# Kernel optimization log

Hardware: AMD Instinct MI355X
Metric: run time of the kernel (lower is better)

The kernel has to match this reference:

```python
import jax, jax.numpy as jnp
import numpy as np

N = 20000      # nodes
E = 640000     # edges (before self loops)
IN = 256       # in_channels == out_channels (forced by classifier size 4*in)
H1, C1 = 8, 16   # conv1: heads=8, out=16 -> concat 128
H2, C2 = 1, 256  # conv2: heads=1, out=out_channels
B = 4096       # article pairs
NEG_SLOPE = 0.2  # PyG GATv2Conv default negative_slope


def setup_inputs() -> dict:
    key = jax.random.key(0)
    ks = jax.random.split(key, 24)
    s = 0.05
    inp = {
        "gnn_x": jax.random.normal(ks[0], (N, IN), jnp.float32),
        "vanilla_x": jax.random.normal(ks[1], (N, IN), jnp.float32),
        "edge_src": jax.random.randint(ks[2], (E,), 0, N, jnp.int32),
        "edge_dst": jax.random.randint(ks[3], (E,), 0, N, jnp.int32),
        "a1_idx": jax.random.randint(ks[4], (B,), 0, N, jnp.int64),
        "a2_idx": jax.random.randint(ks[5], (B,), 0, N, jnp.int64),
        # conv1 params (lin_l, lin_r, att, bias)
        "Wl1": jax.random.normal(ks[6], (IN, H1 * C1), jnp.float32) * s,
        "bl1": jnp.zeros((H1 * C1,), jnp.float32),
        "Wr1": jax.random.normal(ks[7], (IN, H1 * C1), jnp.float32) * s,
        "br1": jnp.zeros((H1 * C1,), jnp.float32),
        "att1": jax.random.normal(ks[8], (H1, C1), jnp.float32) * s,
        "bias1": jnp.zeros((H1 * C1,), jnp.float32),
        # conv2 params
        "Wl2": jax.random.normal(ks[9], (H1 * C1, H2 * C2), jnp.float32) * s,
        "bl2": jnp.zeros((H2 * C2,), jnp.float32),
        "Wr2": jax.random.normal(ks[10], (H1 * C1, H2 * C2), jnp.float32) * s,
        "br2": jnp.zeros((H2 * C2,), jnp.float32),
        "att2": jax.random.normal(ks[11], (H2, C2), jnp.float32) * s,
        "bias2": jnp.zeros((H2 * C2,), jnp.float32),
        # classifier
        "Wc": jax.random.normal(ks[12], (4 * IN, 1), jnp.float32) * s,
        "bc": jnp.zeros((1,), jnp.float32),
    }
    return inp


def _gatv2_layer(x, src, dst, Wl, bl, Wr, br, att, bias):
    """GATv2Conv: x_l = lin_l(x)[src], x_r = lin_r(x)[dst];
    e = att . leaky_relu(x_l + x_r); segment softmax over dst; scatter-add x_l*alpha."""
    n = x.shape[0]
    h, c = att.shape
    xl = (x @ Wl + bl).reshape(n, h, c)
    xr = (x @ Wr + br).reshape(n, h, c)
    # per-edge attention logits [E, H]
    e = jnp.einsum('ehc,hc->eh', jax.nn.leaky_relu(xl[src] + xr[dst], NEG_SLOPE), att)
    # segment softmax over destination nodes (self loops guarantee non-empty segments)
    emax = jax.ops.segment_max(e, dst, num_segments=n)
    ex = jnp.exp(e - emax[dst])
    denom = jax.ops.segment_sum(ex, dst, num_segments=n)
    alpha = ex / denom[dst]                      # [E, H]
    out = jax.ops.segment_sum(alpha[:, :, None] * xl[src], dst, num_segments=n)  # [N,H,C]
    return out.reshape(n, h * c) + bias          # concat=True (heads=1 identical)


def reference(gnn_x, vanilla_x, Wl1, bl1, Wr1, br1, att1, bias1,
              Wl2, bl2, Wr2, br2, att2, bias2, Wc, bc,
              edge_src, edge_dst, a1_idx, a2_idx):
    n = gnn_x.shape[0]
    loops = jnp.arange(n, dtype=edge_src.dtype)
    src = jnp.concatenate([edge_src, loops])     # PyG add_self_loops=True
    dst = jnp.concatenate([edge_dst, loops])
    x = _gatv2_layer(gnn_x, src, dst, Wl1, bl1, Wr1, br1, att1, bias1)
    x = jax.nn.relu(x)
    x = _gatv2_layer(x, src, dst, Wl2, bl2, Wr2, br2, att2, bias2)
    combined = jnp.concatenate(
        [vanilla_x[a1_idx], vanilla_x[a2_idx], x[a1_idx], x[a2_idx]], axis=1)  # [B, 4*IN]
    logits = combined @ Wc + bc                  # [B, 1]
    return logits
```

## Files before the change

kernel.cpp:

```cpp
#include <hip/hip_runtime.h>
#include <math.h>

#define N_NODES 20000
#define M_PAD   20032
#define E_EDGES 640000
#define ET (E_EDGES + N_NODES)
#define IN_CH 256
#define D1 128
#define D2 256
#define BPAIRS 4096
#define NEG 0.2f
#define LOG2E 1.4426950408889634f

#define NB_HIST   128
#define CHUNK     ((ET + NB_HIST - 1) / NB_HIST)
#define HALF_BINS 10000

#define WT_BLOCKS    32
#define ZC_BLOCKS    20
#define XCONV_BLOCKS (M_PAD * IN_CH / 4 / 4 / 256)
#define PREP_BLOCKS  (NB_HIST + WT_BLOCKS + ZC_BLOCKS + XCONV_BLOCKS)

#define RP_BLOCKS ((N_NODES + 255) / 256)

#define G1X (M_PAD / 64)
#define G1Y (D1 / 64)
#define G1_BLOCKS (G1X * G1Y)
#define SCAT_BLOCKS ((ET + 255) / 256)

#if __has_builtin(__builtin_amdgcn_exp2f)
#define EXP2F(x) __builtin_amdgcn_exp2f(x)
#else
#define EXP2F(x) exp2f(x)
#endif

typedef __bf16 bf16x8 __attribute__((ext_vector_type(8)));
typedef float  f32x4  __attribute__((ext_vector_type(4)));
typedef float  f32x2  __attribute__((ext_vector_type(2)));
typedef unsigned short u16x4 __attribute__((ext_vector_type(4)));

__device__ __forceinline__ unsigned short f2b(float f) {
    unsigned int u = __float_as_uint(f);
    unsigned int r = u + 0x7FFFu + ((u >> 16) & 1u);
    return (unsigned short)(r >> 16);
}
__device__ __forceinline__ unsigned char f2f8(float f) {
    return (unsigned char)(__builtin_amdgcn_cvt_pk_fp8_f32(f, f, 0, false) & 0xFF);
}
template <bool HI>
__device__ __forceinline__ f32x2 f8up2(unsigned int u) {
    return __builtin_amdgcn_cvt_pk_f32_fp8((int)u, HI);
}
__device__ __forceinline__ f32x2 up2(unsigned int u) {
    f32x2 r;
    r.x = __uint_as_float(u << 16);
    r.y = __uint_as_float(u & 0xFFFF0000u);
    return r;
}
__device__ __forceinline__ f32x2 lrelu2(f32x2 s) {
    return __builtin_elementwise_max(s, s * NEG);
}
__device__ __forceinline__ float lrelu(float s) { return fmaxf(s, NEG * s); }

__device__ __forceinline__ void unpack8(uint4 u, float* v) {
    v[0] = __uint_as_float(u.x << 16); v[1] = __uint_as_float(u.x & 0xFFFF0000u);
    v[2] = __uint_as_float(u.y << 16); v[3] = __uint_as_float(u.y & 0xFFFF0000u);
    v[4] = __uint_as_float(u.z << 16); v[5] = __uint_as_float(u.z & 0xFFFF0000u);
    v[6] = __uint_as_float(u.w << 16); v[7] = __uint_as_float(u.w & 0xFFFF0000u);
}
__device__ __forceinline__ void unpack8_f8(uint2 u, float* v) {
    f32x2 a = f8up2<false>(u.x), b = f8up2<true>(u.x);
    f32x2 c = f8up2<false>(u.y), d = f8up2<true>(u.y);
    v[0] = a.x; v[1] = a.y; v[2] = b.x; v[3] = b.y;
    v[4] = c.x; v[5] = c.y; v[6] = d.x; v[7] = d.y;
}


__global__ __launch_bounds__(256) void prep_kernel(
        const float* __restrict__ gnn_x,
        const float* __restrict__ Wl1, const float* __restrict__ Wr1,
        const float* __restrict__ Wl2, const float* __restrict__ Wr2,
        const int* __restrict__ edge_dst,
        unsigned short* __restrict__ xb,
        unsigned short* __restrict__ wt1l, unsigned short* __restrict__ wt1r,
        unsigned short* __restrict__ wt2l, unsigned short* __restrict__ wt2r,
        int* __restrict__ cb,
        int* __restrict__ rank,
        int* __restrict__ ibuf) {
    __shared__ int lc[HALF_BINS];
    int bid = blockIdx.x;
    if (bid < NB_HIST) {
        int ebeg = bid * CHUNK;
        int eend = min(ebeg + CHUNK, ET);
#pragma unroll 1
        for (int half = 0; half < 2; half++) {
            int lo = half * HALF_BINS;
            for (int i = threadIdx.x; i < HALF_BINS; i += 256) lc[i] = 0;
            __syncthreads();
            for (int e = ebeg + threadIdx.x; e < eend; e += 256) {
                int dst = (e < E_EDGES) ? edge_dst[e] : (e - E_EDGES);
                int d = dst - lo;
                if (0 <= d && d < HALF_BINS) rank[e] = atomicAdd(&lc[d], 1);
            }
            __syncthreads();
            for (int i = threadIdx.x; i < HALF_BINS; i += 256)
                cb[(size_t)bid * N_NODES + lo + i] = lc[i];
            __syncthreads();
        }
    } else if (bid < NB_HIST + WT_BLOCKS) {
        unsigned short* tile = (unsigned short*)lc;
        int t = bid - NB_HIST;
        int m = t >> 3;
        int tt = t & 7;
        const float* W;
        unsigned short* Wt;
        int K, N;
        if (m == 0)      { W = Wl1; Wt = wt1l; K = IN_CH; N = D1; }
        else if (m == 1) { W = Wr1; Wt = wt1r; K = IN_CH; N = D1; }
        else if (m == 2) { W = Wl2; Wt = wt2l; K = D1; N = D2; }
        else             { W = Wr2; Wt = wt2r; K = D1; N = D2; }
        int ntn = N >> 6;
        int k0 = (tt / ntn) << 6;
        int n0 = (tt % ntn) << 6;
        int c = threadIdx.x & 63;
        int rr = threadIdx.x >> 6;
#pragma unroll
        for (int ch = 0; ch < 16; ch++) {
            int row = rr * 16 + ch;
            tile[row * 65 + c] = f2b(W[(size_t)(k0 + row) * N + n0 + c]);
        }
        __syncthreads();
#pragma unroll
        for (int ch = 0; ch < 16; ch++) {
            int n = rr * 16 + ch;
            Wt[(size_t)(n0 + n) * K + k0 + c] = tile[c * 65 + n];
        }
    } else if (bid < NB_HIST + WT_BLOCKS + ZC_BLOCKS) {
        int q = (bid - NB_HIST - WT_BLOCKS) * 256 + threadIdx.x;
        int4 z; z.x = z.y = z.z = z.w = 0;
        ((int4*)ibuf)[q] = z;
    } else {
        int tid = (bid - NB_HIST - WT_BLOCKS - ZC_BLOCKS) * 256 + threadIdx.x;
        const int NQ = M_PAD * IN_CH / 4;
        int q0 = tid * 4;
#pragma unroll
        for (int j = 0; j < 4; j++) {
            int qi = q0 + j;
            if (qi >= NQ) break;
            int e0 = qi * 4;
            int row = e0 >> 8;
            u16x4 o;
            if (row < N_NODES) {
                f32x4 v = __builtin_nontemporal_load((const f32x4*)(gnn_x + e0));
                o.x = f2b(v.x); o.y = f2b(v.y); o.z = f2b(v.z); o.w = f2b(v.w);
            } else {
                o.x = o.y = o.z = o.w = 0;
            }
            *(u16x4*)(xb + e0) = o;
        }
    }
}

__device__ __forceinline__ void scan256(const int* __restrict__ count,
                                        int* __restrict__ offsets,
                                        int* wbuf) {
    const int PER = 79;
    int t = threadIdx.x;
    int base = t * PER;
    int v[PER];
#pragma unroll
    for (int i = 0; i < PER; i++) {
        int idx = base + i;
        v[i] = (idx < N_NODES) ? count[idx] : 0;
    }
    int sum = 0;
#pragma unroll
    for (int i = 0; i < PER; i++) sum += v[i];
    int lane = t & 63, wave = t >> 6;
    int s = sum;
#pragma unroll
    for (int off = 1; off < 64; off <<= 1) {
        int x = __shfl_up(s, off);
        if (lane >= off) s += x;
    }
    int* wsum = wbuf;
    int* wpre = wbuf + 4;
    if (lane == 63) wsum[wave] = s;
    __syncthreads();
    if (t == 0) {
        int acc = 0;
        for (int w = 0; w < 4; w++) { wpre[w] = acc; acc += wsum[w]; }
    }
    __syncthreads();
    int excl = wpre[wave] + (s - sum);
    if (t == 255) offsets[N_NODES] = excl + sum;
    int run = excl;
#pragma unroll
    for (int i = 0; i < PER; i++) {
        int idx = base + i;
        if (idx < N_NODES) { offsets[idx] = run; run += v[i]; }
    }
}


__global__ __launch_bounds__(256) void repprefix_scan_kernel(
        int* __restrict__ cb, int* __restrict__ count,
        int* __restrict__ done, int* __restrict__ offsets) {
    __shared__ int wbuf[8];
    __shared__ int islast;
    int dst = blockIdx.x * 256 + threadIdx.x;
    if (dst < N_NODES) {
        int v[NB_HIST];
#pragma unroll
        for (int r = 0; r < NB_HIST; r++)
            v[r] = cb[(size_t)r * N_NODES + dst];
        int run = 0;
#pragma unroll
        for (int r = 0; r < NB_HIST; r++) {
            int c = v[r];
            v[r] = run;
            run += c;
        }
#pragma unroll
        for (int r = 0; r < NB_HIST; r++)
            cb[(size_t)r * N_NODES + dst] = v[r];
        atomicAdd(&count[dst], run);
    }
    __builtin_amdgcn_s_waitcnt(0);
    __syncthreads();
    if (threadIdx.x == 0) {
        int old = __hip_atomic_fetch_add(done, 1, __ATOMIC_RELAXED,
                                         __HIP_MEMORY_SCOPE_AGENT);
        islast = (old == RP_BLOCKS - 1) ? 1 : 0;
    }
    __syncthreads();
    if (islast) {
        scan256(count, offsets, wbuf);
    }
}


template <int K>
__device__ __forceinline__ void dual_gemm_tile(
        const unsigned short* __restrict__ A,
        const unsigned short* __restrict__ Wtl,
        const unsigned short* __restrict__ Wtr,
        const float* __restrict__ bl, const float* __restrict__ br,
        unsigned char* __restrict__ Yl, unsigned short* __restrict__ Yr,
        int M, int NOUT, int bx, int by) {
    const int NK = K / 32;
    int wave = threadIdx.x >> 6;
    int lane = threadIdx.x & 63;
    int row0 = bx * 64;
    int col0 = (by * 4 + wave) * 16;
    int rsub = lane & 15;
    int koff = (lane >> 4) * 8;

    const unsigned short* ap  = A   + (size_t)(row0 + rsub) * K + koff;
    const unsigned short* bpl = Wtl + (size_t)(col0 + rsub) * K + koff;
    const unsigned short* bpr = Wtr + (size_t)(col0 + rsub) * K + koff;

    bf16x8 bfl[NK], bfr[NK];
#pragma unroll
    for (int kb = 0; kb < NK; kb++) {
        bfl[kb] = *(const bf16x8*)(bpl + kb * 32);
        bfr[kb] = *(const bf16x8*)(bpr + kb * 32);
    }

    f32x4 l0 = {0.f, 0.f, 0.f, 0.f};
    f32x4 l1 = l0, l2 = l0, l3 = l0, r0 = l0, r1 = l0, r2 = l0, r3 = l0;

#pragma unroll
    for (int kb = 0; kb < NK; kb++) {
        int off = kb * 32;
        bf16x8 a0 = *(const bf16x8*)(ap + off);
        bf16x8 a1 = *(const bf16x8*)(ap + 16 * K + off);
        bf16x8 a2 = *(const bf16x8*)(ap + 32 * K + off);
        bf16x8 a3 = *(const bf16x8*)(ap + 48 * K + off);
        l0 = __builtin_amdgcn_mfma_f32_16x16x32_bf16(a0, bfl[kb], l0, 0, 0, 0);
        r0 = __builtin_amdgcn_mfma_f32_16x16x32_bf16(a0, bfr[kb], r0, 0, 0, 0);
        l1 = __builtin_amdgcn_mfma_f32_16x16x32_bf16(a1, bfl[kb], l1, 0, 0, 0);
        r1 = __builtin_amdgcn_mfma_f32_16x16x32_bf16(a1, bfr[kb], r1, 0, 0, 0);
        l2 = __builtin_amdgcn_mfma_f32_16x16x32_bf16(a2, bfl[kb], l2, 0, 0, 0);
        r2 = __builtin_amdgcn_mfma_f32_16x16x32_bf16(a2, bfr[kb], r2, 0, 0, 0);
        l3 = __builtin_amdgcn_mfma_f32_16x16x32_bf16(a3, bfl[kb], l3, 0, 0, 0);
        r3 = __builtin_amdgcn_mfma_f32_16x16x32_bf16(a3, bfr[kb], r3, 0, 0, 0);
    }

    int colg = col0 + rsub;
    float bvl = bl[colg];
    float bvr = br[colg];
    int rbase = row0 + (lane >> 4) * 4;
#pragma unroll
    for (int t = 0; t < 4; t++) {
        f32x4 al = (t == 0) ? l0 : (t == 1) ? l1 : (t == 2) ? l2 : l3;
        f32x4 ar = (t == 0) ? r0 : (t == 1) ? r1 : (t == 2) ? r2 : r3;
#pragma unroll
        for (int r = 0; r < 4; r++) {
            int row = rbase + t * 16 + r;
            if (row < M) {
                Yl[(size_t)row * NOUT + colg] = f2f8(al[r] + bvl);
                Yr[(size_t)row * NOUT + colg] = f2b(ar[r] + bvr);
            }
        }
    }
}


__global__ __launch_bounds__(256) void gemm1_scatter_kernel(
        const unsigned short* __restrict__ A,
        const unsigned short* __restrict__ Wtl,
        const unsigned short* __restrict__ Wtr,
        const float* __restrict__ bl, const float* __restrict__ br,
        unsigned char* __restrict__ Yl, unsigned short* __restrict__ Yr,
        const int* __restrict__ edge_src, const int* __restrict__ edge_dst,
        const int* __restrict__ rank, const int* __restrict__ offsets,
        const int* __restrict__ cb, int* __restrict__ sorted_src) {
    int bid = blockIdx.x;
    if (bid < G1_BLOCKS) {
        dual_gemm_tile<IN_CH>(A, Wtl, Wtr, bl, br, Yl, Yr,
                              N_NODES, D1, bid % G1X, bid / G1X);
    } else {
        int e = (bid - G1_BLOCKS) * 256 + threadIdx.x;
        if (e >= ET) return;
        int dst = (e < E_EDGES) ? edge_dst[e] : (e - E_EDGES);
        int src = (e < E_EDGES) ? edge_src[e] : (e - E_EDGES);
        int rep = e / CHUNK;
        sorted_src[offsets[dst] + cb[(size_t)rep * N_NODES + dst] + rank[e]] = src;
    }
}


__global__ __launch_bounds__(256) void aggregate1_kernel(
        const unsigned char* __restrict__ xl1, const unsigned short* __restrict__ xr1,
        const float* __restrict__ att1, const float* __restrict__ bias1,
        const int* __restrict__ offsets, const int* __restrict__ sorted_src,
        unsigned short* __restrict__ x1) {
    int wave = threadIdx.x >> 6;
    int lane = threadIdx.x & 63;
    int q = lane >> 4;
    int ql = lane & 15;
    int dst = blockIdx.x * 4 + wave;
    if (dst >= M_PAD) return;
    int c0 = ql * 8;
    if (dst >= N_NODES) {
        if (q == 0) {
            uint4 z; z.x = z.y = z.z = z.w = 0;
            *(uint4*)(x1 + (size_t)dst * D1 + c0) = z;
        }
        return;
    }

    uint4 xu = *(const uint4*)(xr1 + (size_t)dst * D1 + c0);
    f32x2 xr[4] = {up2(xu.x), up2(xu.y), up2(xu.z), up2(xu.w)};
    float4 aa0 = *(const float4*)(att1 + c0);
    float4 aa1 = *(const float4*)(att1 + c0 + 4);
    f32x2 att[4];
    att[0].x = aa0.x * LOG2E; att[0].y = aa0.y * LOG2E;
    att[1].x = aa0.z * LOG2E; att[1].y = aa0.w * LOG2E;
    att[2].x = aa1.x * LOG2E; att[2].y = aa1.y * LOG2E;
    att[3].x = aa1.z * LOG2E; att[3].y = aa1.w * LOG2E;

    int beg = offsets[dst], end = offsets[dst + 1];
    const unsigned char* base = xl1 + c0;

    float l = 0.f;
    f32x2 acc[4] = {{0.f,0.f},{0.f,0.f},{0.f,0.f},{0.f,0.f}};

    int i = beg;
    int s0 = sorted_src[min(i + q, end - 1)];
    uint2 g0 = *(const uint2*)(base + (size_t)s0 * D1);
    bool more1 = (i + 4) < end;
    uint2 g1;
    if (more1) {
        int s1 = sorted_src[min(i + 4 + q, end - 1)];
        g1 = *(const uint2*)(base + (size_t)s1 * D1);
    }
    while (true) {
        bool more2 = (i + 8) < end;
        uint2 g2;
        if (more2) {
            int s2 = sorted_src[min(i + 8 + q, end - 1)];
            g2 = *(const uint2*)(base + (size_t)s2 * D1);
        }
        bool act = (i + q) < end;
        f32x2 v0 = f8up2<false>(g0.x), v1 = f8up2<true>(g0.x);
        f32x2 v2 = f8up2<false>(g0.y), v3 = f8up2<true>(g0.y);
        f32x2 p2 = att[0] * lrelu2(v0 + xr[0]);
        p2 += att[1] * lrelu2(v1 + xr[1]);
        p2 += att[2] * lrelu2(v2 + xr[2]);
        p2 += att[3] * lrelu2(v3 + xr[3]);
        float p = p2.x + p2.y;
        p += __shfl_xor(p, 1);
        float w = act ? EXP2F(p) : 0.f;
        l += w;
        acc[0] += w * v0; acc[1] += w * v1; acc[2] += w * v2; acc[3] += w * v3;
        if (!more1) break;
        i += 4;
        g0 = g1; g1 = g2; more1 = more2;
    }
    l += __shfl_xor(l, 16);
    l += __shfl_xor(l, 32);
#pragma unroll
    for (int j = 0; j < 4; j++) {
        f32x2 t;
        t.x = __shfl_xor(acc[j].x, 16); t.y = __shfl_xor(acc[j].y, 16);
        acc[j] += t;
        t.x = __shfl_xor(acc[j].x, 32); t.y = __shfl_xor(acc[j].y, 32);
        acc[j] += t;
    }
    if (q == 0) {
        float inv = 1.f / l;
        float4 bb0 = *(const float4*)(bias1 + c0);
        float4 bb1 = *(const float4*)(bias1 + c0 + 4);
        unsigned short o[8];
        o[0] = f2b(fmaxf(acc[0].x * inv + bb0.x, 0.f));
        o[1] = f2b(fmaxf(acc[0].y * inv + bb0.y, 0.f));
        o[2] = f2b(fmaxf(acc[1].x * inv + bb0.z, 0.f));
        o[3] = f2b(fmaxf(acc[1].y * inv + bb0.w, 0.f));
        o[4] = f2b(fmaxf(acc[2].x * inv + bb1.x, 0.f));
        o[5] = f2b(fmaxf(acc[2].y * inv + bb1.y, 0.f));
        o[6] = f2b(fmaxf(acc[3].x * inv + bb1.z, 0.f));
        o[7] = f2b(fmaxf(acc[3].y * inv + bb1.w, 0.f));
        uint4 ov;
        ov.x = (unsigned int)o[0] | ((unsigned int)o[1] << 16);
        ov.y = (unsigned int)o[2] | ((unsigned int)o[3] << 16);
        ov.z = (unsigned int)o[4] | ((unsigned int)o[5] << 16);
        ov.w = (unsigned int)o[6] | ((unsigned int)o[7] << 16);
        *(uint4*)(x1 + (size_t)dst * D1 + c0) = ov;
    }
}


template <int K>
__global__ __launch_bounds__(256) void dual_gemm_w32_kernel(
        const unsigned short* __restrict__ A,
        const unsigned short* __restrict__ Wtl,
        const unsigned short* __restrict__ Wtr,
        const float* __restrict__ bl, const float* __restrict__ br,
        unsigned char* __restrict__ Yl, unsigned short* __restrict__ Yr,
        int M, int NOUT) {
    const int NK = K / 32;
    int wave = threadIdx.x >> 6;
    int lane = threadIdx.x & 63;
    int row0 = blockIdx.x * 64;
    int col0 = blockIdx.y * 128 + wave * 32;
    int rsub = lane & 15;
    int koff = (lane >> 4) * 8;

    const unsigned short* ap = A + (size_t)(row0 + rsub) * K + koff;

    bf16x8 bfl[2][NK], bfr[2][NK];
#pragma unroll
    for (int c = 0; c < 2; c++) {
        const unsigned short* bpl = Wtl + (size_t)(col0 + c * 16 + rsub) * K + koff;
        const unsigned short* bpr = Wtr + (size_t)(col0 + c * 16 + rsub) * K + koff;
#pragma unroll
        for (int kb = 0; kb < NK; kb++) {
            bfl[c][kb] = *(const bf16x8*)(bpl + kb * 32);
            bfr[c][kb] = *(const bf16x8*)(bpr + kb * 32);
        }
    }

    f32x4 accl[2][4], accr[2][4];
#pragma unroll
    for (int c = 0; c < 2; c++)
#pragma unroll
        for (int t = 0; t < 4; t++) {
            accl[c][t] = (f32x4){0.f, 0.f, 0.f, 0.f};
            accr[c][t] = (f32x4){0.f, 0.f, 0.f, 0.f};
        }

#pragma unroll
    for (int kb = 0; kb < NK; kb++) {
        int off = kb * 32;
        bf16x8 a[4];
        a[0] = *(const bf16x8*)(ap + off);
        a[1] = *(const bf16x8*)(ap + 16 * K + off);
        a[2] = *(const bf16x8*)(ap + 32 * K + off);
        a[3] = *(const bf16x8*)(ap + 48 * K + off);
#pragma unroll
        for (int t = 0; t < 4; t++) {
#pragma unroll
            for (int c = 0; c < 2; c++) {
                accl[c][t] = __builtin_amdgcn_mfma_f32_16x16x32_bf16(
                    a[t], bfl[c][kb], accl[c][t], 0, 0, 0);
                accr[c][t] = __builtin_amdgcn_mfma_f32_16x16x32_bf16(
                    a[t], bfr[c][kb], accr[c][t], 0, 0, 0);
            }
        }
    }

    int rbase = row0 + (lane >> 4) * 4;
#pragma unroll
    for (int c = 0; c < 2; c++) {
        int colg = col0 + c * 16 + rsub;
        float bvl = bl[colg];
        float bvr = br[colg];
#pragma unroll
        for (int t = 0; t < 4; t++) {
#pragma unroll
            for (int r = 0; r < 4; r++) {
                int row = rbase + t * 16 + r;
                if (row < M) {
                    Yl[(size_t)row * NOUT + colg] = f2f8(accl[c][t][r] + bvl);
                    Yr[(size_t)row * NOUT + colg] = f2b(accr[c][t][r] + bvr);
                }
            }
        }
    }
}


__global__ __launch_bounds__(256) void agg2_classifier_kernel(
        const unsigned char* __restrict__ xl2, const unsigned short* __restrict__ xr2,
        const float* __restrict__ att2, const float* __restrict__ bias2,
        const int* __restrict__ offsets, const int* __restrict__ sorted_src,
        const float* __restrict__ vanilla_x,
        const int* __restrict__ a1_raw, const int* __restrict__ a2_raw,
        const float* __restrict__ Wc, const float* __restrict__ bc,
        float* __restrict__ out) {
    __shared__ float x2row[2][D2];
    __shared__ float mrg[2][32][9];
    __shared__ float part[4];
    __shared__ int stride_s;
    int t = threadIdx.x;
    if (t < 64) {
        bool z = (t < 31) ? (a1_raw[1 + 2 * t] == 0) : true;
        unsigned long long m = __ballot(z);
        if (t == 0) stride_s = (m == ~0ull) ? 2 : 1;
    }
    __syncthreads();
    int stride = stride_s;
    int b = blockIdx.x;
    int a1 = a1_raw[(long)b * stride];
    int a2 = a2_raw[(long)b * stride];

    int wave = t >> 6;
    int d = wave >> 1;
    int ww = wave & 1;
    int lane = t & 63;
    int half = lane >> 5;
    int hl = lane & 31;
    int c0 = hl * 8;
    int dst = d ? a2 : a1;

    float xr[8], att[8];
    unpack8(*(const uint4*)(xr2 + (size_t)dst * D2 + c0), xr);
#pragma unroll
    for (int j = 0; j < 8; j++) att[j] = att2[c0 + j] * LOG2E;
    int beg = offsets[dst], end = offsets[dst + 1];
    const unsigned char* base = xl2 + c0;

    float l = 0.f;
    float acc[8];
#pragma unroll
    for (int j = 0; j < 8; j++) acc[j] = 0.f;

    int sub = 2 * ww + half;
    int i = beg;
    int s0 = sorted_src[min(i + sub, end - 1)];
    uint2 g0 = *(const uint2*)(base + (size_t)s0 * D2);
    bool more1 = (i + 4) < end;
    uint2 g1;
    if (more1) {
        int s1 = sorted_src[min(i + 4 + sub, end - 1)];
        g1 = *(const uint2*)(base + (size_t)s1 * D2);
    }
    while (true) {
        bool more2 = (i + 8) < end;
        uint2 g2;
        if (more2) {
            int s2 = sorted_src[min(i + 8 + sub, end - 1)];
            g2 = *(const uint2*)(base + (size_t)s2 * D2);
        }
        bool act = (i + sub) < end;
        float v[8];
        unpack8_f8(g0, v);
        float p = 0.f;
#pragma unroll
        for (int j = 0; j < 8; j++) p = fmaf(att[j], lrelu(v[j] + xr[j]), p);
        p += __shfl_xor(p, 1);
        p += __shfl_xor(p, 2);
        p += __shfl_xor(p, 4);
        p += __shfl_xor(p, 8);
        p += __shfl_xor(p, 16);
        float w = act ? EXP2F(p) : 0.f;
        l += w;
#pragma unroll
        for (int j = 0; j < 8; j++) acc[j] += w * v[j];
        if (!more1) break;
        i += 4;
        g0 = g1; g1 = g2; more1 = more2;
    }
    l += __shfl_xor(l, 32);
#pragma unroll
    for (int j = 0; j < 8; j++) acc[j] += __shfl_xor(acc[j], 32);
    if (ww == 1 && half == 0) {
        mrg[d][hl][0] = l;
#pragma unroll
        for (int j = 0; j < 8; j++) mrg[d][hl][1 + j] = acc[j];
    }
    __syncthreads();
    if (ww == 0 && half == 0) {
        l += mrg[d][hl][0];
#pragma unroll
        for (int j = 0; j < 8; j++) acc[j] += mrg[d][hl][1 + j];
        float inv = 1.f / l;
#pragma unroll
        for (int j = 0; j < 8; j++)
            x2row[d][c0 + j] = acc[j] * inv + bias2[c0 + j];
    }
    __syncthreads();

    float s = vanilla_x[(size_t)a1 * IN_CH + t] * Wc[t]
            + vanilla_x[(size_t)a2 * IN_CH + t] * Wc[IN_CH + t]
            + x2row[0][t] * Wc[2 * IN_CH + t]
            + x2row[1][t] * Wc[3 * IN_CH + t];
    s += __shfl_xor(s, 1);
    s += __shfl_xor(s, 2);
    s += __shfl_xor(s, 4);
    s += __shfl_xor(s, 8);
    s += __shfl_xor(s, 16);
    s += __shfl_xor(s, 32);
    if (lane == 0) part[wave] = s;
    __syncthreads();
    if (t == 0) out[b] = part[0] + part[1] + part[2] + part[3] + bc[0];
}


extern "C" void kernel_launch(void* const* d_in, const int* in_sizes, int n_in,
                              void* d_out, int out_size, void* d_ws, size_t ws_size,
                              hipStream_t stream) {
    const float* gnn_x     = (const float*)d_in[0];
    const float* vanilla_x = (const float*)d_in[1];
    const int*   edge_src  = (const int*)d_in[2];
    const int*   edge_dst  = (const int*)d_in[3];
    const int*   a1_idx    = (const int*)d_in[4];
    const int*   a2_idx    = (const int*)d_in[5];
    const float* Wl1   = (const float*)d_in[6];
    const float* bl1   = (const float*)d_in[7];
    const float* Wr1   = (const float*)d_in[8];
    const float* br1   = (const float*)d_in[9];
    const float* att1  = (const float*)d_in[10];
    const float* bias1 = (const float*)d_in[11];
    const float* Wl2   = (const float*)d_in[12];
    const float* bl2   = (const float*)d_in[13];
    const float* Wr2   = (const float*)d_in[14];
    const float* br2   = (const float*)d_in[15];
    const float* att2  = (const float*)d_in[16];
    const float* bias2 = (const float*)d_in[17];
    const float* Wc    = (const float*)d_in[18];
    const float* bc    = (const float*)d_in[19];
    float* out = (float*)d_out;

    char* p = (char*)d_ws;
    unsigned short* xb   = (unsigned short*)p; p += (size_t)M_PAD * IN_CH * 2;
    unsigned short* x1b  = (unsigned short*)p; p += (size_t)M_PAD * D1 * 2;
    unsigned char*  xl1b = (unsigned char*)p;  p += (size_t)N_NODES * D1;
    unsigned short* xr1b = (unsigned short*)p; p += (size_t)N_NODES * D1 * 2;
    unsigned char*  xl2b = (unsigned char*)p;  p += (size_t)N_NODES * D2;
    unsigned short* xr2b = (unsigned short*)p; p += (size_t)N_NODES * D2 * 2;
    unsigned short* wt1l = (unsigned short*)p; p += (size_t)D1 * IN_CH * 2;
    unsigned short* wt1r = (unsigned short*)p; p += (size_t)D1 * IN_CH * 2;
    unsigned short* wt2l = (unsigned short*)p; p += (size_t)D2 * D1 * 2;
    unsigned short* wt2r = (unsigned short*)p; p += (size_t)D2 * D1 * 2;
    int* ibuf       = (int*)p; p += (size_t)20480 * 4;
    int* offsets    = (int*)p; p += (size_t)(N_NODES + 4) * 4;
    int* rank       = (int*)p; p += (size_t)ET * 4;
    int* sorted_src = (int*)p; p += (size_t)ET * 4;
    int* cb         = (int*)p; p += (size_t)NB_HIST * N_NODES * 4;
    int* count = ibuf;
    int* done  = ibuf + 20032;

    prep_kernel<<<PREP_BLOCKS, 256, 0, stream>>>(
        gnn_x, Wl1, Wr1, Wl2, Wr2, edge_dst,
        xb, wt1l, wt1r, wt2l, wt2r, cb, rank, ibuf);

    repprefix_scan_kernel<<<RP_BLOCKS, 256, 0, stream>>>(
        cb, count, done, offsets);

    gemm1_scatter_kernel<<<G1_BLOCKS + SCAT_BLOCKS, 256, 0, stream>>>(
        xb, wt1l, wt1r, bl1, br1, xl1b, xr1b,
        edge_src, edge_dst, rank, offsets, cb, sorted_src);

    aggregate1_kernel<<<M_PAD / 4, 256, 0, stream>>>(
        xl1b, xr1b, att1, bias1, offsets, sorted_src, x1b);

    dim3 g2(M_PAD / 64, D2 / 128);
    dual_gemm_w32_kernel<D1><<<g2, 256, 0, stream>>>(
        x1b, wt2l, wt2r, bl2, br2, xl2b, xr2b, N_NODES, D2);

    agg2_classifier_kernel<<<BPAIRS, 256, 0, stream>>>(
        xl2b, xr2b, att2, bias2, offsets, sorted_src,
        vanilla_x, a1_idx, a2_idx, Wc, bc, out);
}
```

Measured before the change: 256.3 us.

## Split histogram halves across blocks and use two waves per node in aggregate1

The histogram phase of the prep kernel now gives each half of the destination bin range its own block, which doubles the block count and removes the serial two-pass loop. The layer-1 aggregation now assigns two waves to each destination node. Each wave processes an interleaved half of the edges, and the partial sums are merged through shared memory after a block barrier. Both changes expose more parallelism and shorten the per-node dependency chain. The cost is that edge_dst is read twice across blocks, plus extra shared-memory traffic and a __syncthreads in the aggregation.

```diff
diff --git a/kernel.cpp b/kernel.cpp
--- a/kernel.cpp
+++ b/kernel.cpp
@@ -15,11 +15,12 @@
 #define NB_HIST   128
 #define CHUNK     ((ET + NB_HIST - 1) / NB_HIST)
 #define HALF_BINS 10000
+#define HIST_BLOCKS (NB_HIST * 2)
 
 #define WT_BLOCKS    32
 #define ZC_BLOCKS    20
 #define XCONV_BLOCKS (M_PAD * IN_CH / 4 / 4 / 256)
-#define PREP_BLOCKS  (NB_HIST + WT_BLOCKS + ZC_BLOCKS + XCONV_BLOCKS)
+#define PREP_BLOCKS  (HIST_BLOCKS + WT_BLOCKS + ZC_BLOCKS + XCONV_BLOCKS)
 
 #define RP_BLOCKS ((N_NODES + 255) / 256)
 
@@ -89,27 +90,25 @@
         int* __restrict__ ibuf) {
     __shared__ int lc[HALF_BINS];
     int bid = blockIdx.x;
-    if (bid < NB_HIST) {
-        int ebeg = bid * CHUNK;
+    if (bid < HIST_BLOCKS) {
+        int chunk = bid >> 1;
+        int half  = bid & 1;
+        int ebeg = chunk * CHUNK;
         int eend = min(ebeg + CHUNK, ET);
-#pragma unroll 1
-        for (int half = 0; half < 2; half++) {
-            int lo = half * HALF_BINS;
-            for (int i = threadIdx.x; i < HALF_BINS; i += 256) lc[i] = 0;
-            __syncthreads();
-            for (int e = ebeg + threadIdx.x; e < eend; e += 256) {
-                int dst = (e < E_EDGES) ? edge_dst[e] : (e - E_EDGES);
-                int d = dst - lo;
-                if (0 <= d && d < HALF_BINS) rank[e] = atomicAdd(&lc[d], 1);
-            }
-            __syncthreads();
-            for (int i = threadIdx.x; i < HALF_BINS; i += 256)
-                cb[(size_t)bid * N_NODES + lo + i] = lc[i];
-            __syncthreads();
-        }
-    } else if (bid < NB_HIST + WT_BLOCKS) {
+        int lo = half * HALF_BINS;
+        for (int i = threadIdx.x; i < HALF_BINS; i += 256) lc[i] = 0;
+        __syncthreads();
+        for (int e = ebeg + threadIdx.x; e < eend; e += 256) {
+            int dst = (e < E_EDGES) ? edge_dst[e] : (e - E_EDGES);
+            int d = dst - lo;
+            if (0 <= d && d < HALF_BINS) rank[e] = atomicAdd(&lc[d], 1);
+        }
+        __syncthreads();
+        for (int i = threadIdx.x; i < HALF_BINS; i += 256)
+            cb[(size_t)chunk * N_NODES + lo + i] = lc[i];
+    } else if (bid < HIST_BLOCKS + WT_BLOCKS) {
         unsigned short* tile = (unsigned short*)lc;
-        int t = bid - NB_HIST;
+        int t = bid - HIST_BLOCKS;
         int m = t >> 3;
         int tt = t & 7;
         const float* W;
@@ -135,12 +134,12 @@
             int n = rr * 16 + ch;
             Wt[(size_t)(n0 + n) * K + k0 + c] = tile[c * 65 + n];
         }
-    } else if (bid < NB_HIST + WT_BLOCKS + ZC_BLOCKS) {
-        int q = (bid - NB_HIST - WT_BLOCKS) * 256 + threadIdx.x;
+    } else if (bid < HIST_BLOCKS + WT_BLOCKS + ZC_BLOCKS) {
+        int q = (bid - HIST_BLOCKS - WT_BLOCKS) * 256 + threadIdx.x;
         int4 z; z.x = z.y = z.z = z.w = 0;
         ((int4*)ibuf)[q] = z;
     } else {
-        int tid = (bid - NB_HIST - WT_BLOCKS - ZC_BLOCKS) * 256 + threadIdx.x;
+        int tid = (bid - HIST_BLOCKS - WT_BLOCKS - ZC_BLOCKS) * 256 + threadIdx.x;
         const int NQ = M_PAD * IN_CH / 4;
         int q0 = tid * 4;
 #pragma unroll
@@ -336,80 +335,100 @@
         const float* __restrict__ att1, const float* __restrict__ bias1,
         const int* __restrict__ offsets, const int* __restrict__ sorted_src,
         unsigned short* __restrict__ x1) {
+    __shared__ float mrg[2][16][9];
     int wave = threadIdx.x >> 6;
     int lane = threadIdx.x & 63;
+    int ds = wave >> 1;
+    int w  = wave & 1;
     int q = lane >> 4;
     int ql = lane & 15;
-    int dst = blockIdx.x * 4 + wave;
-    if (dst >= M_PAD) return;
+    int dst = blockIdx.x * 2 + ds;
     int c0 = ql * 8;
-    if (dst >= N_NODES) {
-        if (q == 0) {
+    bool pad = (dst >= N_NODES);
+
+    float l = 0.f;
+    f32x2 acc[4] = {{0.f,0.f},{0.f,0.f},{0.f,0.f},{0.f,0.f}};
+
+    if (!pad) {
+        uint4 xu = *(const uint4*)(xr1 + (size_t)dst * D1 + c0);
+        f32x2 xr[4] = {up2(xu.x), up2(xu.y), up2(xu.z), up2(xu.w)};
+        float4 aa0 = *(const float4*)(att1 + c0);
+        float4 aa1 = *(const float4*)(att1 + c0 + 4);
+        f32x2 att[4];
+        att[0].x = aa0.x * LOG2E; att[0].y = aa0.y * LOG2E;
+        att[1].x = aa0.z * LOG2E; att[1].y = aa0.w * LOG2E;
+        att[2].x = aa1.x * LOG2E; att[2].y = aa1.y * LOG2E;
+        att[3].x = aa1.z * LOG2E; att[3].y = aa1.w * LOG2E;
+
+        int beg = offsets[dst], end = offsets[dst + 1];
+        const unsigned char* base = xl1 + c0;
+        int slot = 4 * w + q;
+
+        int i = beg;
+        int s0 = sorted_src[min(i + slot, end - 1)];
+        uint2 g0 = *(const uint2*)(base + (size_t)s0 * D1);
+        bool more1 = (i + 8) < end;
+        uint2 g1;
+        if (more1) {
+            int s1 = sorted_src[min(i + 8 + slot, end - 1)];
+            g1 = *(const uint2*)(base + (size_t)s1 * D1);
+        }
+        while (true) {
+            bool more2 = (i + 16) < end;
+            uint2 g2;
+            if (more2) {
+                int s2 = sorted_src[min(i + 16 + slot, end - 1)];
+                g2 = *(const uint2*)(base + (size_t)s2 * D1);
+            }
+            bool act = (i + slot) < end;
+            f32x2 v0 = f8up2<false>(g0.x), v1 = f8up2<true>(g0.x);
+            f32x2 v2 = f8up2<false>(g0.y), v3 = f8up2<true>(g0.y);
+            f32x2 p2 = att[0] * lrelu2(v0 + xr[0]);
+            p2 += att[1] * lrelu2(v1 + xr[1]);
+            p2 += att[2] * lrelu2(v2 + xr[2]);
+            p2 += att[3] * lrelu2(v3 + xr[3]);
+            float p = p2.x + p2.y;
+            p += __shfl_xor(p, 1);
+            float wgt = act ? EXP2F(p) : 0.f;
+            l += wgt;
+            acc[0] += wgt * v0; acc[1] += wgt * v1;
+            acc[2] += wgt * v2; acc[3] += wgt * v3;
+            if (!more1) break;
+            i += 8;
+            g0 = g1; g1 = g2; more1 = more2;
+        }
+        l += __shfl_xor(l, 16);
+        l += __shfl_xor(l, 32);
+#pragma unroll
+        for (int j = 0; j < 4; j++) {
+            f32x2 t;
+            t.x = __shfl_xor(acc[j].x, 16); t.y = __shfl_xor(acc[j].y, 16);
+            acc[j] += t;
+            t.x = __shfl_xor(acc[j].x, 32); t.y = __shfl_xor(acc[j].y, 32);
+            acc[j] += t;
+        }
+        if (w == 1 && q == 0) {
+            mrg[ds][ql][0] = l;
+#pragma unroll
+            for (int j = 0; j < 4; j++) {
+                mrg[ds][ql][1 + 2 * j] = acc[j].x;
+                mrg[ds][ql][2 + 2 * j] = acc[j].y;
+            }
+        }
+    }
+    __syncthreads();
+    if (w == 0 && q == 0) {
+        if (pad) {
             uint4 z; z.x = z.y = z.z = z.w = 0;
             *(uint4*)(x1 + (size_t)dst * D1 + c0) = z;
-        }
-        return;
-    }
-
-    uint4 xu = *(const uint4*)(xr1 + (size_t)dst * D1 + c0);
-    f32x2 xr[4] = {up2(xu.x), up2(xu.y), up2(xu.z), up2(xu.w)};
-    float4 aa0 = *(const float4*)(att1 + c0);
-    float4 aa1 = *(const float4*)(att1 + c0 + 4);
-    f32x2 att[4];
-    att[0].x = aa0.x * LOG2E; att[0].y = aa0.y * LOG2E;
-    att[1].x = aa0.z * LOG2E; att[1].y = aa0.w * LOG2E;
-    att[2].x = aa1.x * LOG2E; att[2].y = aa1.y * LOG2E;
-    att[3].x = aa1.z * LOG2E; att[3].y = aa1.w * LOG2E;
-
-    int beg = offsets[dst], end = offsets[dst + 1];
-    const unsigned char* base = xl1 + c0;
-
-    float l = 0.f;
-    f32x2 acc[4] = {{0.f,0.f},{0.f,0.f},{0.f,0.f},{0.f,0.f}};
-
-    int i = beg;
-    int s0 = sorted_src[min(i + q, end - 1)];
-    uint2 g0 = *(const uint2*)(base + (size_t)s0 * D1);
-    bool more1 = (i + 4) < end;
-    uint2 g1;
-    if (more1) {
-        int s1 = sorted_src[min(i + 4 + q, end - 1)];
-        g1 = *(const uint2*)(base + (size_t)s1 * D1);
-    }
-    while (true) {
-        bool more2 = (i + 8) < end;
-        uint2 g2;
-        if (more2) {
-            int s2 = sorted_src[min(i + 8 + q, end - 1)];
-            g2 = *(const uint2*)(base + (size_t)s2 * D1);
-        }
-        bool act = (i + q) < end;
-        f32x2 v0 = f8up2<false>(g0.x), v1 = f8up2<true>(g0.x);
-        f32x2 v2 = f8up2<false>(g0.y), v3 = f8up2<true>(g0.y);
-        f32x2 p2 = att[0] * lrelu2(v0 + xr[0]);
-        p2 += att[1] * lrelu2(v1 + xr[1]);
-        p2 += att[2] * lrelu2(v2 + xr[2]);
-        p2 += att[3] * lrelu2(v3 + xr[3]);
-        float p = p2.x + p2.y;
-        p += __shfl_xor(p, 1);
-        float w = act ? EXP2F(p) : 0.f;
-        l += w;
-        acc[0] += w * v0; acc[1] += w * v1; acc[2] += w * v2; acc[3] += w * v3;
-        if (!more1) break;
-        i += 4;
-        g0 = g1; g1 = g2; more1 = more2;
-    }
-    l += __shfl_xor(l, 16);
-    l += __shfl_xor(l, 32);
-#pragma unroll
-    for (int j = 0; j < 4; j++) {
-        f32x2 t;
-        t.x = __shfl_xor(acc[j].x, 16); t.y = __shfl_xor(acc[j].y, 16);
-        acc[j] += t;
-        t.x = __shfl_xor(acc[j].x, 32); t.y = __shfl_xor(acc[j].y, 32);
-        acc[j] += t;
-    }
-    if (q == 0) {
+            return;
+        }
+        l += mrg[ds][ql][0];
+#pragma unroll
+        for (int j = 0; j < 4; j++) {
+            acc[j].x += mrg[ds][ql][1 + 2 * j];
+            acc[j].y += mrg[ds][ql][2 + 2 * j];
+        }
         float inv = 1.f / l;
         float4 bb0 = *(const float4*)(bias1 + c0);
         float4 bb1 = *(const float4*)(bias1 + c0 + 4);
@@ -684,7 +703,7 @@
         xb, wt1l, wt1r, bl1, br1, xl1b, xr1b,
         edge_src, edge_dst, rank, offsets, cb, sorted_src);
 
-    aggregate1_kernel<<<M_PAD / 4, 256, 0, stream>>>(
+    aggregate1_kernel<<<M_PAD / 2, 256, 0, stream>>>(
         xl1b, xr1b, att1, bias1, offsets, sorted_src, x1b);
 
     dim3 g2(M_PAD / 64, D2 / 128);
```

Measured after the change: 253.1 us. Within noise of the previous version (-1.2%).
